# Kernel tuning notes

Hardware: AMD Instinct MI355X
Metric: run time of the kernel (lower is better)

Reference implementation:

```python
import jax, jax.numpy as jnp
import numpy as np

N, E, G = 50000, 800000, 64
D, DE, DIN, L = 64, 4, 11, 2


def _lin(x, w, b):
    return x @ w + b


def _bn(x, g, b, eps=1e-5):
    # BatchNorm1d in training mode: biased batch statistics over dim 0
    m = x.mean(0)
    v = x.var(0)
    return (x - m) * jax.lax.rsqrt(v + eps) * g + b


def setup_inputs() -> dict:
    key = jax.random.key(0)
    ks = iter(jax.random.split(key, 64))

    def rn(shape, s=0.05):
        return jax.random.normal(next(ks), shape, jnp.float32) * s

    inp = dict(
        x=rn((N, DIN), 1.0),
        pos=rn((N, 3), 1.0),
        edge_attr=rn((E, DE), 1.0),
        edge_index=jax.random.randint(next(ks), (2, E), 0, N),
        batch=jnp.sort(jax.random.randint(next(ks), (N,), 0, G)),
        lin_in_w=rn((DIN, D)), lin_in_b=jnp.zeros((D,), jnp.float32),
        lin_pred_w=rn((D, 1)), lin_pred_b=jnp.zeros((1,), jnp.float32),
        # per-layer stacked params (leading dim L)
        msg_w1=rn((L, 2 * D + DE + 1, D)), msg_b1=jnp.zeros((L, D), jnp.float32),
        msg_g1=jnp.ones((L, D), jnp.float32), msg_be1=jnp.zeros((L, D), jnp.float32),
        msg_w2=rn((L, D, D)), msg_b2=jnp.zeros((L, D), jnp.float32),
        msg_g2=jnp.ones((L, D), jnp.float32), msg_be2=jnp.zeros((L, D), jnp.float32),
        pos_w1=rn((L, D, D)), pos_b1=jnp.zeros((L, D), jnp.float32),
        pos_g=jnp.ones((L, D), jnp.float32), pos_be=jnp.zeros((L, D), jnp.float32),
        pos_w2=rn((L, D, 1)), pos_b2=jnp.zeros((L, 1), jnp.float32),
        upd_w1=rn((L, 2 * D, D)), upd_b1=jnp.zeros((L, D), jnp.float32),
        upd_g1=jnp.ones((L, D), jnp.float32), upd_be1=jnp.zeros((L, D), jnp.float32),
        upd_w2=rn((L, D, D)), upd_b2=jnp.zeros((L, D), jnp.float32),
        upd_g2=jnp.ones((L, D), jnp.float32), upd_be2=jnp.zeros((L, D), jnp.float32),
    )
    return inp


def reference(x, pos, edge_attr, edge_index, batch,
              lin_in_w, lin_in_b, lin_pred_w, lin_pred_b,
              msg_w1, msg_b1, msg_g1, msg_be1, msg_w2, msg_b2, msg_g2, msg_be2,
              pos_w1, pos_b1, pos_g, pos_be, pos_w2, pos_b2,
              upd_w1, upd_b1, upd_g1, upd_be1, upd_w2, upd_b2, upd_g2, upd_be2):
    src, dst = edge_index[0], edge_index[1]  # h_j = h[src], h_i = h[dst]
    h = x @ lin_in_w + lin_in_b
    p = pos
    deg = jnp.maximum(jax.ops.segment_sum(jnp.ones((E,), h.dtype), dst, N), 1.0)
    for l in range(L):
        h_i, h_j = h[dst], h[src]          # (E, D) gathers
        pd = p[dst] - p[src]               # (E, 3)
        radial = jnp.sum(pd * pd, axis=1, keepdims=True)  # (E, 1)
        m = jnp.concatenate([h_i, h_j, radial, edge_attr], -1)  # (E, 2D+DE+1)
        m = jax.nn.relu(_bn(_lin(m, msg_w1[l], msg_b1[l]), msg_g1[l], msg_be1[l]))
        m = jax.nn.relu(_bn(_lin(m, msg_w2[l], msg_b2[l]), msg_g2[l], msg_be2[l]))
        s = jax.nn.relu(_bn(_lin(m, pos_w1[l], pos_b1[l]), pos_g[l], pos_be[l]))
        s = _lin(s, pos_w2[l], pos_b2[l])  # (E, 1) scalar gate
        pos_upd = pd * s                   # (E, 3)
        m_aggr = jax.ops.segment_sum(m, dst, N)                    # sum aggr
        p_aggr = jax.ops.segment_sum(pos_upd, dst, N) / deg[:, None]  # mean aggr
        u = jnp.concatenate([h, m_aggr], -1)
        u = jax.nn.relu(_bn(_lin(u, upd_w1[l], upd_b1[l]), upd_g1[l], upd_be1[l]))
        u = jax.nn.relu(_bn(_lin(u, upd_w2[l], upd_b2[l]), upd_g2[l], upd_be2[l]))
        h = h + u          # residual on node features (MPNNModel style)
        p = p + p_aggr     # position update from layer
    cnt = jnp.maximum(jax.ops.segment_sum(jnp.ones((N,), h.dtype), batch, G), 1.0)
    h_graph = jax.ops.segment_sum(h, batch, G) / cnt[:, None]  # global_mean_pool
    out = h_graph @ lin_pred_w + lin_pred_b
    return out.reshape(-1)
```

## Files before the change

### kernel.cpp

```cpp
#include <hip/hip_runtime.h>

#define Nn 50000
#define Ee 800000
#define Gg 64
#define Dd 64
#define KIN 133
#define ES 68
#define EPS 1e-5f


__global__ __launch_bounds__(256) void k_lin_in(const float* __restrict__ x,
    const float* __restrict__ W, const float* __restrict__ B, float* __restrict__ h)
{
    __shared__ float Ws[11 * 64];
    __shared__ float Bs[64];
    int t = threadIdx.x;
    for (int i = t; i < 11 * 64; i += 256) Ws[i] = W[i];
    if (t < 64) Bs[t] = B[t];
    __syncthreads();
    int i = blockIdx.x * 256 + t;
    if (i < Nn * 64) {
        int n = i >> 6, c = i & 63;
        float acc = Bs[c];
        #pragma unroll
        for (int k = 0; k < 11; k++) acc += x[n * 11 + k] * Ws[k * 64 + c];
        h[i] = acc;
    }
}

__global__ __launch_bounds__(256) void k_deg(const int* __restrict__ ei, float* __restrict__ deg)
{
    int e = blockIdx.x * 256 + threadIdx.x;
    if (e < Ee) atomicAdd(&deg[ei[Ee + e]], 1.f);
}

__global__ __launch_bounds__(256) void k_cnt(const int* __restrict__ batch, float* __restrict__ cnt)
{
    int n = blockIdx.x * 256 + threadIdx.x;
    if (n < Nn) atomicAdd(&cnt[batch[n]], 1.f);
}


__global__ __launch_bounds__(256) void k_edge_lin1(
    const float* __restrict__ h, const float* __restrict__ p,
    const float* __restrict__ ea, const int* __restrict__ ei,
    const float* __restrict__ W, const float* __restrict__ B,
    float* __restrict__ ybuf, float* __restrict__ stats_out)
{
    __shared__ float Ws[KIN * 64];
    __shared__ float Bs[64];
    __shared__ float in_t[KIN * ES];
    int t = threadIdx.x;
    for (int i = t; i < KIN * 64; i += 256) Ws[i] = W[i];
    if (t < 64) Bs[t] = B[t];
    int tx = t & 15, ty = t >> 4;
    int c = t & 63, eg = t >> 6;
    float ssum[4] = {0, 0, 0, 0}, ssq[4] = {0, 0, 0, 0};
    for (int tile = blockIdx.x; tile < Ee / 64; tile += gridDim.x) {
        int te = tile * 64;
        __syncthreads();
        for (int e = eg; e < 64; e += 4) {
            int sr = ei[te + e], ds = ei[Ee + te + e];
            in_t[c * ES + e]        = h[(size_t)ds * 64 + c];
            in_t[(64 + c) * ES + e] = h[(size_t)sr * 64 + c];
        }
        if (t < 64) {
            int e = t;
            int sr = ei[te + e], ds = ei[Ee + te + e];
            float dx = p[ds * 3 + 0] - p[sr * 3 + 0];
            float dy = p[ds * 3 + 1] - p[sr * 3 + 1];
            float dz = p[ds * 3 + 2] - p[sr * 3 + 2];
            in_t[128 * ES + e] = dx * dx + dy * dy + dz * dz;
            float4 a4 = *(const float4*)&ea[(size_t)(te + e) * 4];
            in_t[129 * ES + e] = a4.x;
            in_t[130 * ES + e] = a4.y;
            in_t[131 * ES + e] = a4.z;
            in_t[132 * ES + e] = a4.w;
        }
        __syncthreads();
        float acc[4][4];
        #pragma unroll
        for (int i = 0; i < 4; i++)
            #pragma unroll
            for (int j = 0; j < 4; j++) acc[i][j] = Bs[4 * ty + j];
        for (int k = 0; k < KIN; k++) {
            float av[4], wv[4];
            *(float4*)av = *(const float4*)&in_t[k * ES + 4 * tx];
            *(float4*)wv = *(const float4*)&Ws[k * 64 + 4 * ty];
            #pragma unroll
            for (int i = 0; i < 4; i++)
                #pragma unroll
                for (int j = 0; j < 4; j++)
                    acc[i][j] += av[i] * wv[j];
        }
        #pragma unroll
        for (int i = 0; i < 4; i++) {
            size_t e = (size_t)te + 4 * tx + i;
            float4 o; o.x = acc[i][0]; o.y = acc[i][1]; o.z = acc[i][2]; o.w = acc[i][3];
            *(float4*)&ybuf[e * 64 + 4 * ty] = o;
            #pragma unroll
            for (int j = 0; j < 4; j++) { ssum[j] += acc[i][j]; ssq[j] += acc[i][j] * acc[i][j]; }
        }
    }
    #pragma unroll
    for (int j = 0; j < 4; j++) {
        float s = ssum[j], q = ssq[j];
        #pragma unroll
        for (int o2 = 1; o2 < 16; o2 <<= 1) { s += __shfl_xor(s, o2); q += __shfl_xor(q, o2); }
        if (tx == 0) {
            atomicAdd(&stats_out[4 * ty + j], s);
            atomicAdd(&stats_out[64 + 4 * ty + j], q);
        }
    }
}


template<int AGGR>
__global__ __launch_bounds__(256) void k_edge_lin64(
    const float* __restrict__ stats_in, const float* __restrict__ gg,
    const float* __restrict__ be,
    const float* __restrict__ W, const float* __restrict__ B,
    const int* __restrict__ ei, float* __restrict__ magg,
    float* __restrict__ ybuf, float* __restrict__ stats_out)
{
    __shared__ float Ws[64 * 64];
    __shared__ float As[64], Cs[64], Bs[64];
    __shared__ float in_t[64 * ES];
    int t = threadIdx.x;
    if (t < 64) {
        float mean = stats_in[t] * (1.f / Ee);
        float var  = stats_in[64 + t] * (1.f / Ee) - mean * mean;
        float a = gg[t] * rsqrtf(var + EPS);
        As[t] = a; Cs[t] = be[t] - mean * a; Bs[t] = B[t];
    }
    for (int i = t; i < 64 * 64; i += 256) Ws[i] = W[i];
    int tx = t & 15, ty = t >> 4;
    int c = t & 63, eg = t >> 6;
    float ssum[4] = {0, 0, 0, 0}, ssq[4] = {0, 0, 0, 0};
    for (int tile = blockIdx.x; tile < Ee / 64; tile += gridDim.x) {
        int te = tile * 64;
        __syncthreads();
        for (int e = eg; e < 64; e += 4) {
            float y = ybuf[(size_t)(te + e) * 64 + c];
            in_t[c * ES + e] = fmaxf(As[c] * y + Cs[c], 0.f);
        }
        __syncthreads();
        float acc[4][4];
        #pragma unroll
        for (int i = 0; i < 4; i++)
            #pragma unroll
            for (int j = 0; j < 4; j++) acc[i][j] = Bs[4 * ty + j];
        for (int k = 0; k < 64; k++) {
            float av[4], wv[4];
            *(float4*)av = *(const float4*)&in_t[k * ES + 4 * tx];
            *(float4*)wv = *(const float4*)&Ws[k * 64 + 4 * ty];
            #pragma unroll
            for (int i = 0; i < 4; i++)
                #pragma unroll
                for (int j = 0; j < 4; j++)
                    acc[i][j] += av[i] * wv[j];
        }
        if (AGGR) {
            for (int e = eg; e < 64; e += 4) {
                int ds = ei[Ee + te + e];
                atomicAdd(&magg[(size_t)ds * 64 + c], in_t[c * ES + e]);
            }
        }
        #pragma unroll
        for (int i = 0; i < 4; i++) {
            size_t e = (size_t)te + 4 * tx + i;
            float4 o; o.x = acc[i][0]; o.y = acc[i][1]; o.z = acc[i][2]; o.w = acc[i][3];
            *(float4*)&ybuf[e * 64 + 4 * ty] = o;
            #pragma unroll
            for (int j = 0; j < 4; j++) { ssum[j] += acc[i][j]; ssq[j] += acc[i][j] * acc[i][j]; }
        }
    }
    #pragma unroll
    for (int j = 0; j < 4; j++) {
        float s = ssum[j], q = ssq[j];
        #pragma unroll
        for (int o2 = 1; o2 < 16; o2 <<= 1) { s += __shfl_xor(s, o2); q += __shfl_xor(q, o2); }
        if (tx == 0) {
            atomicAdd(&stats_out[4 * ty + j], s);
            atomicAdd(&stats_out[64 + 4 * ty + j], q);
        }
    }
}


__global__ __launch_bounds__(256) void k_pos2(
    const float* __restrict__ stats_in, const float* __restrict__ gg, const float* __restrict__ be,
    const float* __restrict__ W2, const float* __restrict__ B2,
    const float* __restrict__ p, const int* __restrict__ ei,
    const float* __restrict__ ybuf, float* __restrict__ pagg)
{
    __shared__ float As[64], Cs[64], Ws[64];
    int t = threadIdx.x;
    if (t < 64) {
        float mean = stats_in[t] * (1.f / Ee);
        float var  = stats_in[64 + t] * (1.f / Ee) - mean * mean;
        float a = gg[t] * rsqrtf(var + EPS);
        As[t] = a; Cs[t] = be[t] - mean * a; Ws[t] = W2[t];
    }
    __syncthreads();
    int e = blockIdx.x * 256 + t;
    if (e >= Ee) return;
    float acc = B2[0];
    const float* row = &ybuf[(size_t)e * 64];
    #pragma unroll
    for (int u = 0; u < 16; u++) {
        float4 y = *(const float4*)&row[4 * u];
        acc += fmaxf(As[4 * u + 0] * y.x + Cs[4 * u + 0], 0.f) * Ws[4 * u + 0]
             + fmaxf(As[4 * u + 1] * y.y + Cs[4 * u + 1], 0.f) * Ws[4 * u + 1]
             + fmaxf(As[4 * u + 2] * y.z + Cs[4 * u + 2], 0.f) * Ws[4 * u + 2]
             + fmaxf(As[4 * u + 3] * y.w + Cs[4 * u + 3], 0.f) * Ws[4 * u + 3];
    }
    int sr = ei[e], ds = ei[Ee + e];
    float dx = p[ds * 3 + 0] - p[sr * 3 + 0];
    float dy = p[ds * 3 + 1] - p[sr * 3 + 1];
    float dz = p[ds * 3 + 2] - p[sr * 3 + 2];
    atomicAdd(&pagg[ds * 3 + 0], dx * acc);
    atomicAdd(&pagg[ds * 3 + 1], dy * acc);
    atomicAdd(&pagg[ds * 3 + 2], dz * acc);
}


__global__ __launch_bounds__(256) void k_node_lin1(
    const float* __restrict__ h, const float* __restrict__ magg,
    const float* __restrict__ W, const float* __restrict__ B,
    float* __restrict__ yn, float* __restrict__ stats_out)
{
    __shared__ float Ws[128 * 64];
    __shared__ float Bs[64];
    __shared__ float in_t[128 * ES];
    int t = threadIdx.x;
    for (int i = t; i < 128 * 64; i += 256) Ws[i] = W[i];
    if (t < 64) Bs[t] = B[t];
    int tx = t & 15, ty = t >> 4, c = t & 63, eg = t >> 6;
    float ssum[4] = {0, 0, 0, 0}, ssq[4] = {0, 0, 0, 0};
    int nT = (Nn + 63) / 64;
    for (int tile = blockIdx.x; tile < nT; tile += gridDim.x) {
        int te = tile * 64;
        __syncthreads();
        for (int e = eg; e < 64; e += 4) {
            int n = te + e;
            bool v = n < Nn;
            in_t[c * ES + e]        = v ? h[(size_t)n * 64 + c]    : 0.f;
            in_t[(64 + c) * ES + e] = v ? magg[(size_t)n * 64 + c] : 0.f;
        }
        __syncthreads();
        float acc[4][4];
        #pragma unroll
        for (int i = 0; i < 4; i++)
            #pragma unroll
            for (int j = 0; j < 4; j++) acc[i][j] = Bs[4 * ty + j];
        for (int k = 0; k < 128; k++) {
            float av[4], wv[4];
            *(float4*)av = *(const float4*)&in_t[k * ES + 4 * tx];
            *(float4*)wv = *(const float4*)&Ws[k * 64 + 4 * ty];
            #pragma unroll
            for (int i = 0; i < 4; i++)
                #pragma unroll
                for (int j = 0; j < 4; j++)
                    acc[i][j] += av[i] * wv[j];
        }
        #pragma unroll
        for (int i = 0; i < 4; i++) {
            int n = te + 4 * tx + i;
            if (n < Nn) {
                float4 o; o.x = acc[i][0]; o.y = acc[i][1]; o.z = acc[i][2]; o.w = acc[i][3];
                *(float4*)&yn[(size_t)n * 64 + 4 * ty] = o;
                #pragma unroll
                for (int j = 0; j < 4; j++) { ssum[j] += acc[i][j]; ssq[j] += acc[i][j] * acc[i][j]; }
            }
        }
    }
    #pragma unroll
    for (int j = 0; j < 4; j++) {
        float s = ssum[j], q = ssq[j];
        #pragma unroll
        for (int o2 = 1; o2 < 16; o2 <<= 1) { s += __shfl_xor(s, o2); q += __shfl_xor(q, o2); }
        if (tx == 0) {
            atomicAdd(&stats_out[4 * ty + j], s);
            atomicAdd(&stats_out[64 + 4 * ty + j], q);
        }
    }
}


__global__ __launch_bounds__(256) void k_node_lin64(
    const float* __restrict__ stats_in, const float* __restrict__ gg, const float* __restrict__ be,
    const float* __restrict__ W, const float* __restrict__ B,
    float* __restrict__ yn, float* __restrict__ stats_out)
{
    __shared__ float Ws[64 * 64];
    __shared__ float As[64], Cs[64], Bs[64];
    __shared__ float in_t[64 * ES];
    int t = threadIdx.x;
    if (t < 64) {
        float mean = stats_in[t] * (1.f / Nn);
        float var  = stats_in[64 + t] * (1.f / Nn) - mean * mean;
        float a = gg[t] * rsqrtf(var + EPS);
        As[t] = a; Cs[t] = be[t] - mean * a; Bs[t] = B[t];
    }
    for (int i = t; i < 64 * 64; i += 256) Ws[i] = W[i];
    int tx = t & 15, ty = t >> 4, c = t & 63, eg = t >> 6;
    float ssum[4] = {0, 0, 0, 0}, ssq[4] = {0, 0, 0, 0};
    int nT = (Nn + 63) / 64;
    for (int tile = blockIdx.x; tile < nT; tile += gridDim.x) {
        int te = tile * 64;
        __syncthreads();
        for (int e = eg; e < 64; e += 4) {
            int n = te + e;
            float y = (n < Nn) ? yn[(size_t)n * 64 + c] : 0.f;
            in_t[c * ES + e] = fmaxf(As[c] * y + Cs[c], 0.f);
        }
        __syncthreads();
        float acc[4][4];
        #pragma unroll
        for (int i = 0; i < 4; i++)
            #pragma unroll
            for (int j = 0; j < 4; j++) acc[i][j] = Bs[4 * ty + j];
        for (int k = 0; k < 64; k++) {
            float av[4], wv[4];
            *(float4*)av = *(const float4*)&in_t[k * ES + 4 * tx];
            *(float4*)wv = *(const float4*)&Ws[k * 64 + 4 * ty];
            #pragma unroll
            for (int i = 0; i < 4; i++)
                #pragma unroll
                for (int j = 0; j < 4; j++)
                    acc[i][j] += av[i] * wv[j];
        }
        #pragma unroll
        for (int i = 0; i < 4; i++) {
            int n = te + 4 * tx + i;
            if (n < Nn) {
                float4 o; o.x = acc[i][0]; o.y = acc[i][1]; o.z = acc[i][2]; o.w = acc[i][3];
                *(float4*)&yn[(size_t)n * 64 + 4 * ty] = o;
                #pragma unroll
                for (int j = 0; j < 4; j++) { ssum[j] += acc[i][j]; ssq[j] += acc[i][j] * acc[i][j]; }
            }
        }
    }
    #pragma unroll
    for (int j = 0; j < 4; j++) {
        float s = ssum[j], q = ssq[j];
        #pragma unroll
        for (int o2 = 1; o2 < 16; o2 <<= 1) { s += __shfl_xor(s, o2); q += __shfl_xor(q, o2); }
        if (tx == 0) {
            atomicAdd(&stats_out[4 * ty + j], s);
            atomicAdd(&stats_out[64 + 4 * ty + j], q);
        }
    }
}


__global__ __launch_bounds__(256) void k_node_update(
    const float* __restrict__ stats_in, const float* __restrict__ gg, const float* __restrict__ be,
    const float* __restrict__ yn, float* __restrict__ h,
    const float* __restrict__ p_in, float* __restrict__ p_out,
    const float* __restrict__ pagg, const float* __restrict__ deg)
{
    int i = blockIdx.x * 256 + threadIdx.x;
    if (i < Nn * 64) {
        int c = i & 63;
        float mean = stats_in[c] * (1.f / Nn);
        float var  = stats_in[64 + c] * (1.f / Nn) - mean * mean;
        float a = gg[c] * rsqrtf(var + EPS);
        float cc = be[c] - mean * a;
        h[i] += fmaxf(a * yn[i] + cc, 0.f);
    }
    if (i < Nn * 3) {
        float dg = fmaxf(deg[i / 3], 1.f);
        p_out[i] = p_in[i] + pagg[i] / dg;
    }
}


__global__ __launch_bounds__(256) void k_pool(const int* __restrict__ batch,
    const float* __restrict__ h, float* __restrict__ pool)
{
    int i = blockIdx.x * 256 + threadIdx.x;
    if (i < Nn * 64) {
        int n = i >> 6, c = i & 63;
        atomicAdd(&pool[(size_t)batch[n] * 64 + c], h[i]);
    }
}

__global__ void k_out(const float* __restrict__ pool, const float* __restrict__ cnt,
    const float* __restrict__ W, const float* __restrict__ B, float* __restrict__ out)
{
    int g = threadIdx.x;
    if (g < 64) {
        float acc = 0.f;
        for (int c = 0; c < 64; c++) acc += pool[g * 64 + c] * W[c];
        out[g] = acc / fmaxf(cnt[g], 1.f) + B[0];
    }
}


extern "C" void kernel_launch(void* const* d_in, const int* in_sizes, int n_in,
                              void* d_out, int out_size, void* d_ws, size_t ws_size,
                              hipStream_t stream)
{
    const float* x        = (const float*)d_in[0];
    const float* pos      = (const float*)d_in[1];
    const float* ea       = (const float*)d_in[2];
    const int*   ei       = (const int*)  d_in[3];
    const int*   batch    = (const int*)  d_in[4];
    const float* lin_in_w = (const float*)d_in[5];
    const float* lin_in_b = (const float*)d_in[6];
    const float* lin_pr_w = (const float*)d_in[7];
    const float* lin_pr_b = (const float*)d_in[8];
    const float* msg_w1   = (const float*)d_in[9];
    const float* msg_b1   = (const float*)d_in[10];
    const float* msg_g1   = (const float*)d_in[11];
    const float* msg_be1  = (const float*)d_in[12];
    const float* msg_w2   = (const float*)d_in[13];
    const float* msg_b2   = (const float*)d_in[14];
    const float* msg_g2   = (const float*)d_in[15];
    const float* msg_be2  = (const float*)d_in[16];
    const float* pos_w1   = (const float*)d_in[17];
    const float* pos_b1   = (const float*)d_in[18];
    const float* pos_g    = (const float*)d_in[19];
    const float* pos_be   = (const float*)d_in[20];
    const float* pos_w2   = (const float*)d_in[21];
    const float* pos_b2   = (const float*)d_in[22];
    const float* upd_w1   = (const float*)d_in[23];
    const float* upd_b1   = (const float*)d_in[24];
    const float* upd_g1   = (const float*)d_in[25];
    const float* upd_be1  = (const float*)d_in[26];
    const float* upd_w2   = (const float*)d_in[27];
    const float* upd_b2   = (const float*)d_in[28];
    const float* upd_g2   = (const float*)d_in[29];
    const float* upd_be2  = (const float*)d_in[30];
    float* out = (float*)d_out;

    float* ws = (float*)d_ws;
    size_t o = 0;
    float* h    = ws + o; o += (size_t)Nn * 64;
    float* ybuf = ws + o; o += (size_t)Ee * 64;
    float* yn   = ws + o; o += (size_t)Nn * 64;
    float* magg = ws + o; o += (size_t)Nn * 64;
    float* pagg = ws + o; o += (size_t)Nn * 3;
    float* pws  = ws + o; o += (size_t)Nn * 3;
    float* stats= ws + o; o += 1280;
    float* pool = ws + o; o += 64 * 64;
    float* cnt  = ws + o; o += 64;
    float* deg  = ws + o; o += Nn;
    if (ws_size < o * sizeof(float)) return;

    hipMemsetAsync(stats, 0, (size_t)(1280 + 64 * 64 + 64 + Nn) * sizeof(float), stream);
    k_lin_in<<<(Nn * 64 + 255) / 256, 256, 0, stream>>>(x, lin_in_w, lin_in_b, h);
    k_deg<<<(Ee + 255) / 256, 256, 0, stream>>>(ei, deg);
    k_cnt<<<(Nn + 255) / 256, 256, 0, stream>>>(batch, cnt);

    for (int l = 0; l < 2; l++) {
        hipMemsetAsync(magg, 0, ((size_t)Nn * 64 + (size_t)Nn * 3) * sizeof(float), stream);
        const float* pc = (l == 0) ? pos : pws;
        float* st = stats + (size_t)l * 5 * 128;
        k_edge_lin1<<<512, 256, 0, stream>>>(h, pc, ea, ei,
            msg_w1 + (size_t)l * KIN * 64, msg_b1 + l * 64, ybuf, st + 0 * 128);
        k_edge_lin64<0><<<1024, 256, 0, stream>>>(st + 0 * 128, msg_g1 + l * 64, msg_be1 + l * 64,
            msg_w2 + (size_t)l * 64 * 64, msg_b2 + l * 64, ei, nullptr, ybuf, st + 1 * 128);
        k_edge_lin64<1><<<1024, 256, 0, stream>>>(st + 1 * 128, msg_g2 + l * 64, msg_be2 + l * 64,
            pos_w1 + (size_t)l * 64 * 64, pos_b1 + l * 64, ei, magg, ybuf, st + 2 * 128);
        k_pos2<<<(Ee + 255) / 256, 256, 0, stream>>>(st + 2 * 128, pos_g + l * 64, pos_be + l * 64,
            pos_w2 + l * 64, pos_b2 + l, pc, ei, ybuf, pagg);
        k_node_lin1<<<782, 256, 0, stream>>>(h, magg,
            upd_w1 + (size_t)l * 128 * 64, upd_b1 + l * 64, yn, st + 3 * 128);
        k_node_lin64<<<782, 256, 0, stream>>>(st + 3 * 128, upd_g1 + l * 64, upd_be1 + l * 64,
            upd_w2 + (size_t)l * 64 * 64, upd_b2 + l * 64, yn, st + 4 * 128);
        k_node_update<<<(Nn * 64 + 255) / 256, 256, 0, stream>>>(st + 4 * 128,
            upd_g2 + l * 64, upd_be2 + l * 64, yn, h, pc, pws, pagg, deg);
    }
    k_pool<<<(Nn * 64 + 255) / 256, 256, 0, stream>>>(batch, h, pool);
    k_out<<<1, 64, 0, stream>>>(pool, cnt, lin_pr_w, lin_pr_b, out);
}
```

Baseline: 2.497 ms.

## Store edge activations as bf16 with ping-pong buffers and swizzled row-major tiles

Edge intermediate activations (E x 64) are now stored in bf16 instead of fp32, which halves the dominant global memory traffic between the edge MLP stages. BN statistics are accumulated from the rounded values. The lin64 kernel now loads tiles row-major with an XOR-swizzled shared layout, applies BN+ReLU while reading from shared memory, and writes into a separate ping-pong buffer. Reduced precision in intermediates risks small numerical deviation from the fp32 reference.

```diff
diff --git a/kernel.cpp b/kernel.cpp
--- a/kernel.cpp
+++ b/kernel.cpp
@@ -2,11 +2,33 @@
 
 #define Nn 50000
 #define Ee 800000
-#define Gg 64
-#define Dd 64
 #define KIN 133
 #define ES 68
 #define EPS 1e-5f
+
+typedef unsigned short u16;
+
+__device__ __forceinline__ u16 f2bf(float f) {
+    union { float f; unsigned u; } v; v.f = f;
+    unsigned r = (v.u + 0x7FFFu + ((v.u >> 16) & 1u)) >> 16;
+    return (u16)r;
+}
+__device__ __forceinline__ float bf2f(u16 s) {
+    union { unsigned u; float f; } v; v.u = ((unsigned)s) << 16;
+    return v.f;
+}
+
+#define BNRELU4(V, A4, C4) \
+    V.x = fmaxf(V.x * A4.x + C4.x, 0.f); \
+    V.y = fmaxf(V.y * A4.y + C4.y, 0.f); \
+    V.z = fmaxf(V.z * A4.z + C4.z, 0.f); \
+    V.w = fmaxf(V.w * A4.w + C4.w, 0.f);
+
+#define FMAROW(ACCI, AV) \
+    ACCI[0] += AV.x * w0.x; ACCI[0] += AV.y * w1.x; ACCI[0] += AV.z * w2.x; ACCI[0] += AV.w * w3.x; \
+    ACCI[1] += AV.x * w0.y; ACCI[1] += AV.y * w1.y; ACCI[1] += AV.z * w2.y; ACCI[1] += AV.w * w3.y; \
+    ACCI[2] += AV.x * w0.z; ACCI[2] += AV.y * w1.z; ACCI[2] += AV.z * w2.z; ACCI[2] += AV.w * w3.z; \
+    ACCI[3] += AV.x * w0.w; ACCI[3] += AV.y * w1.w; ACCI[3] += AV.z * w2.w; ACCI[3] += AV.w * w3.w;
 
 
 __global__ __launch_bounds__(256) void k_lin_in(const float* __restrict__ x,
@@ -45,7 +67,7 @@
     const float* __restrict__ h, const float* __restrict__ p,
     const float* __restrict__ ea, const int* __restrict__ ei,
     const float* __restrict__ W, const float* __restrict__ B,
-    float* __restrict__ ybuf, float* __restrict__ stats_out)
+    u16* __restrict__ yb, float* __restrict__ stats_out)
 {
     __shared__ float Ws[KIN * 64];
     __shared__ float Bs[64];
@@ -96,10 +118,13 @@
         #pragma unroll
         for (int i = 0; i < 4; i++) {
             size_t e = (size_t)te + 4 * tx + i;
-            float4 o; o.x = acc[i][0]; o.y = acc[i][1]; o.z = acc[i][2]; o.w = acc[i][3];
-            *(float4*)&ybuf[e * 64 + 4 * ty] = o;
-            #pragma unroll
-            for (int j = 0; j < 4; j++) { ssum[j] += acc[i][j]; ssq[j] += acc[i][j] * acc[i][j]; }
+            ushort4 o;
+            o.x = f2bf(acc[i][0]); o.y = f2bf(acc[i][1]);
+            o.z = f2bf(acc[i][2]); o.w = f2bf(acc[i][3]);
+            *(ushort4*)&yb[e * 64 + 4 * ty] = o;
+            float r0 = bf2f(o.x), r1 = bf2f(o.y), r2 = bf2f(o.z), r3 = bf2f(o.w);
+            ssum[0] += r0; ssum[1] += r1; ssum[2] += r2; ssum[3] += r3;
+            ssq[0] += r0 * r0; ssq[1] += r1 * r1; ssq[2] += r2 * r2; ssq[3] += r3 * r3;
         }
     }
     #pragma unroll
@@ -121,58 +146,95 @@
     const float* __restrict__ be,
     const float* __restrict__ W, const float* __restrict__ B,
     const int* __restrict__ ei, float* __restrict__ magg,
-    float* __restrict__ ybuf, float* __restrict__ stats_out)
+    const u16* __restrict__ src, u16* __restrict__ dst,
+    float* __restrict__ stats_out)
 {
     __shared__ float Ws[64 * 64];
     __shared__ float As[64], Cs[64], Bs[64];
-    __shared__ float in_t[64 * ES];
+    __shared__ float in_t[64 * 64];
     int t = threadIdx.x;
+    for (int i = t; i < 64 * 64; i += 256) Ws[i] = W[i];
     if (t < 64) {
         float mean = stats_in[t] * (1.f / Ee);
         float var  = stats_in[64 + t] * (1.f / Ee) - mean * mean;
         float a = gg[t] * rsqrtf(var + EPS);
         As[t] = a; Cs[t] = be[t] - mean * a; Bs[t] = B[t];
     }
-    for (int i = t; i < 64 * 64; i += 256) Ws[i] = W[i];
     int tx = t & 15, ty = t >> 4;
-    int c = t & 63, eg = t >> 6;
+    int srow = t >> 4;
+    int sq   = t & 15;
+    int sqp  = 4 * (sq ^ srow);
+    int nt = Ee / 64;
     float ssum[4] = {0, 0, 0, 0}, ssq[4] = {0, 0, 0, 0};
-    for (int tile = blockIdx.x; tile < Ee / 64; tile += gridDim.x) {
+
+    for (int tile = blockIdx.x; tile < nt; tile += gridDim.x) {
         int te = tile * 64;
-        __syncthreads();
-        for (int e = eg; e < 64; e += 4) {
-            float y = ybuf[(size_t)(te + e) * 64 + c];
-            in_t[c * ES + e] = fmaxf(As[c] * y + Cs[c], 0.f);
-        }
-        __syncthreads();
+        ushort4 u0 = *(const ushort4*)&src[(size_t)(te + srow     ) * 64 + 4 * sq];
+        ushort4 u1 = *(const ushort4*)&src[(size_t)(te + srow + 16) * 64 + 4 * sq];
+        ushort4 u2 = *(const ushort4*)&src[(size_t)(te + srow + 32) * 64 + 4 * sq];
+        ushort4 u3 = *(const ushort4*)&src[(size_t)(te + srow + 48) * 64 + 4 * sq];
+        __syncthreads();
+        float4 f;
+        f.x = bf2f(u0.x); f.y = bf2f(u0.y); f.z = bf2f(u0.z); f.w = bf2f(u0.w);
+        *(float4*)&in_t[(srow     ) * 64 + sqp] = f;
+        f.x = bf2f(u1.x); f.y = bf2f(u1.y); f.z = bf2f(u1.z); f.w = bf2f(u1.w);
+        *(float4*)&in_t[(srow + 16) * 64 + sqp] = f;
+        f.x = bf2f(u2.x); f.y = bf2f(u2.y); f.z = bf2f(u2.z); f.w = bf2f(u2.w);
+        *(float4*)&in_t[(srow + 32) * 64 + sqp] = f;
+        f.x = bf2f(u3.x); f.y = bf2f(u3.y); f.z = bf2f(u3.z); f.w = bf2f(u3.w);
+        *(float4*)&in_t[(srow + 48) * 64 + sqp] = f;
+        __syncthreads();
+
         float acc[4][4];
-        #pragma unroll
-        for (int i = 0; i < 4; i++)
-            #pragma unroll
-            for (int j = 0; j < 4; j++) acc[i][j] = Bs[4 * ty + j];
-        for (int k = 0; k < 64; k++) {
-            float av[4], wv[4];
-            *(float4*)av = *(const float4*)&in_t[k * ES + 4 * tx];
-            *(float4*)wv = *(const float4*)&Ws[k * 64 + 4 * ty];
-            #pragma unroll
-            for (int i = 0; i < 4; i++)
-                #pragma unroll
-                for (int j = 0; j < 4; j++)
-                    acc[i][j] += av[i] * wv[j];
+        {
+            float4 b4 = *(const float4*)&Bs[4 * ty];
+            #pragma unroll
+            for (int i = 0; i < 4; i++) {
+                acc[i][0] = b4.x; acc[i][1] = b4.y; acc[i][2] = b4.z; acc[i][3] = b4.w;
+            }
+        }
+        #pragma unroll 4
+        for (int kc = 0; kc < 16; kc++) {
+            int p0 = 4 * (kc ^ tx);
+            float4 a0 = *(const float4*)&in_t[(tx     ) * 64 + p0];
+            float4 a1 = *(const float4*)&in_t[(tx + 16) * 64 + p0];
+            float4 a2 = *(const float4*)&in_t[(tx + 32) * 64 + p0];
+            float4 a3 = *(const float4*)&in_t[(tx + 48) * 64 + p0];
+            float4 as4 = *(const float4*)&As[4 * kc];
+            float4 cs4 = *(const float4*)&Cs[4 * kc];
+            BNRELU4(a0, as4, cs4); BNRELU4(a1, as4, cs4);
+            BNRELU4(a2, as4, cs4); BNRELU4(a3, as4, cs4);
+            float4 w0 = *(const float4*)&Ws[(4 * kc + 0) * 64 + 4 * ty];
+            float4 w1 = *(const float4*)&Ws[(4 * kc + 1) * 64 + 4 * ty];
+            float4 w2 = *(const float4*)&Ws[(4 * kc + 2) * 64 + 4 * ty];
+            float4 w3 = *(const float4*)&Ws[(4 * kc + 3) * 64 + 4 * ty];
+            FMAROW(acc[0], a0); FMAROW(acc[1], a1);
+            FMAROW(acc[2], a2); FMAROW(acc[3], a3);
         }
         if (AGGR) {
-            for (int e = eg; e < 64; e += 4) {
-                int ds = ei[Ee + te + e];
-                atomicAdd(&magg[(size_t)ds * 64 + c], in_t[c * ES + e]);
+            int l = t & 63, w = t >> 6;
+            int dnode = ei[Ee + te + l];
+            #pragma unroll
+            for (int q = 0; q < 4; q++) {
+                int kq = 4 * q + w;
+                float4 v = *(const float4*)&in_t[l * 64 + 4 * (kq ^ (l & 15))];
+                float4 as4 = *(const float4*)&As[4 * kq];
+                float4 cs4 = *(const float4*)&Cs[4 * kq];
+                BNRELU4(v, as4, cs4);
+                float* mg = &magg[(size_t)dnode * 64 + 4 * kq];
+                atomicAdd(mg + 0, v.x); atomicAdd(mg + 1, v.y);
+                atomicAdd(mg + 2, v.z); atomicAdd(mg + 3, v.w);
             }
         }
         #pragma unroll
         for (int i = 0; i < 4; i++) {
-            size_t e = (size_t)te + 4 * tx + i;
-            float4 o; o.x = acc[i][0]; o.y = acc[i][1]; o.z = acc[i][2]; o.w = acc[i][3];
-            *(float4*)&ybuf[e * 64 + 4 * ty] = o;
-            #pragma unroll
-            for (int j = 0; j < 4; j++) { ssum[j] += acc[i][j]; ssq[j] += acc[i][j] * acc[i][j]; }
+            ushort4 o;
+            o.x = f2bf(acc[i][0]); o.y = f2bf(acc[i][1]);
+            o.z = f2bf(acc[i][2]); o.w = f2bf(acc[i][3]);
+            *(ushort4*)&dst[(size_t)(te + tx + 16 * i) * 64 + 4 * ty] = o;
+            float r0 = bf2f(o.x), r1 = bf2f(o.y), r2 = bf2f(o.z), r3 = bf2f(o.w);
+            ssum[0] += r0; ssum[1] += r1; ssum[2] += r2; ssum[3] += r3;
+            ssq[0] += r0 * r0; ssq[1] += r1 * r1; ssq[2] += r2 * r2; ssq[3] += r3 * r3;
         }
     }
     #pragma unroll
@@ -192,7 +254,7 @@
     const float* __restrict__ stats_in, const float* __restrict__ gg, const float* __restrict__ be,
     const float* __restrict__ W2, const float* __restrict__ B2,
     const float* __restrict__ p, const int* __restrict__ ei,
-    const float* __restrict__ ybuf, float* __restrict__ pagg)
+    const u16* __restrict__ yb, float* __restrict__ pagg)
 {
     __shared__ float As[64], Cs[64], Ws[64];
     int t = threadIdx.x;
@@ -204,16 +266,15 @@
     }
     __syncthreads();
     int e = blockIdx.x * 256 + t;
-    if (e >= Ee) return;
+    const u16* row = &yb[(size_t)e * 64];
     float acc = B2[0];
-    const float* row = &ybuf[(size_t)e * 64];
-    #pragma unroll
+    #pragma unroll 4
     for (int u = 0; u < 16; u++) {
-        float4 y = *(const float4*)&row[4 * u];
-        acc += fmaxf(As[4 * u + 0] * y.x + Cs[4 * u + 0], 0.f) * Ws[4 * u + 0]
-             + fmaxf(As[4 * u + 1] * y.y + Cs[4 * u + 1], 0.f) * Ws[4 * u + 1]
-             + fmaxf(As[4 * u + 2] * y.z + Cs[4 * u + 2], 0.f) * Ws[4 * u + 2]
-             + fmaxf(As[4 * u + 3] * y.w + Cs[4 * u + 3], 0.f) * Ws[4 * u + 3];
+        ushort4 y4 = *(const ushort4*)&row[4 * u];
+        acc += fmaxf(As[4 * u + 0] * bf2f(y4.x) + Cs[4 * u + 0], 0.f) * Ws[4 * u + 0]
+             + fmaxf(As[4 * u + 1] * bf2f(y4.y) + Cs[4 * u + 1], 0.f) * Ws[4 * u + 1]
+             + fmaxf(As[4 * u + 2] * bf2f(y4.z) + Cs[4 * u + 2], 0.f) * Ws[4 * u + 2]
+             + fmaxf(As[4 * u + 3] * bf2f(y4.w) + Cs[4 * u + 3], 0.f) * Ws[4 * u + 3];
     }
     int sr = ei[e], ds = ei[Ee + e];
     float dx = p[ds * 3 + 0] - p[sr * 3 + 0];
@@ -439,7 +500,8 @@
     float* ws = (float*)d_ws;
     size_t o = 0;
     float* h    = ws + o; o += (size_t)Nn * 64;
-    float* ybuf = ws + o; o += (size_t)Ee * 64;
+    u16*   ybA  = (u16*)(ws + o); o += (size_t)Ee * 64;
+    u16*   ybB  = ybA + (size_t)Ee * 64;
     float* yn   = ws + o; o += (size_t)Nn * 64;
     float* magg = ws + o; o += (size_t)Nn * 64;
     float* pagg = ws + o; o += (size_t)Nn * 3;
@@ -460,13 +522,13 @@
         const float* pc = (l == 0) ? pos : pws;
         float* st = stats + (size_t)l * 5 * 128;
         k_edge_lin1<<<512, 256, 0, stream>>>(h, pc, ea, ei,
-            msg_w1 + (size_t)l * KIN * 64, msg_b1 + l * 64, ybuf, st + 0 * 128);
+            msg_w1 + (size_t)l * KIN * 64, msg_b1 + l * 64, ybA, st + 0 * 128);
         k_edge_lin64<0><<<1024, 256, 0, stream>>>(st + 0 * 128, msg_g1 + l * 64, msg_be1 + l * 64,
-            msg_w2 + (size_t)l * 64 * 64, msg_b2 + l * 64, ei, nullptr, ybuf, st + 1 * 128);
+            msg_w2 + (size_t)l * 64 * 64, msg_b2 + l * 64, ei, nullptr, ybA, ybB, st + 1 * 128);
         k_edge_lin64<1><<<1024, 256, 0, stream>>>(st + 1 * 128, msg_g2 + l * 64, msg_be2 + l * 64,
-            pos_w1 + (size_t)l * 64 * 64, pos_b1 + l * 64, ei, magg, ybuf, st + 2 * 128);
-        k_pos2<<<(Ee + 255) / 256, 256, 0, stream>>>(st + 2 * 128, pos_g + l * 64, pos_be + l * 64,
-            pos_w2 + l * 64, pos_b2 + l, pc, ei, ybuf, pagg);
+            pos_w1 + (size_t)l * 64 * 64, pos_b1 + l * 64, ei, magg, ybB, ybA, st + 2 * 128);
+        k_pos2<<<Ee / 256, 256, 0, stream>>>(st + 2 * 128, pos_g + l * 64, pos_be + l * 64,
+            pos_w2 + l * 64, pos_b2 + l, pc, ei, ybA, pagg);
         k_node_lin1<<<782, 256, 0, stream>>>(h, magg,
             upd_w1 + (size_t)l * 128 * 64, upd_b1 + l * 64, yn, st + 3 * 128);
         k_node_lin64<<<782, 256, 0, stream>>>(st + 3 * 128, upd_g1 + l * 64, upd_be1 + l * 64,
```

Result: slower. 7.516 ms (+201.0%).
